# Optimization experiments

Measured on AMD Instinct MI355X. Metric: run time of the kernel, lower is better.

The kernel has to match this reference:

```python
import jax, jax.numpy as jnp
import numpy as np

N = 1024      # nodes == subgraphs (NGNN: one subgraph per node)
DEG = 8       # average degree
E = N * DEG   # edges
IND = 32      # indim
OUTD = 32     # outdim


def setup_inputs() -> dict:
    key = jax.random.key(0)
    k0, k1, k2, k3, k4 = jax.random.split(key, 5)
    X = jax.random.normal(k0, (N, N, IND), dtype=jnp.float32)
    # binary tuple-support mask (which (i,j) tuples exist in the sparse 2D tensor)
    mask = jax.random.randint(k1, (N, N), 0, 2).astype(jnp.int32)
    # adjacency edge list: A[row, col] = 1 (structure-only sparse adjacency)
    edge_row = jax.random.randint(k2, (E,), 0, N)  # destination j
    edge_col = jax.random.randint(k3, (E,), 0, N)  # source k
    # MLP (single linear layer, PygHO MLP default)
    W = jax.random.normal(k4, (IND, OUTD), dtype=jnp.float32) / np.sqrt(IND).astype(np.float32)
    b = jnp.zeros((OUTD,), dtype=jnp.float32)
    return {"X": X, "mask": mask, "edge_row": edge_row, "edge_col": edge_col, "W": W, "b": b}


def reference(X, mask, edge_row, edge_col, W, b):
    n = X.shape[0]
    m = mask.astype(X.dtype)[..., None]                      # [n, n, 1]
    # tuplewise MLP on existing tuples: tX[i,j] = X[i,j] @ W + b
    tX = (jnp.einsum("ijd,de->ije", X, W) + b) * m           # [n, n, OUTD]
    # message passing within each subgraph i along node dim j:
    # ret[i, j] = sum_{k : A[j,k]=1} tX[i, k]
    msgs = jnp.take(tX, edge_col, axis=1)                    # [n, E, OUTD] gather sources
    msgs = jnp.moveaxis(msgs, 1, 0)                          # [E, n, OUTD]
    agg = jax.ops.segment_sum(msgs, edge_row, num_segments=n)  # [j, i, OUTD]
    ret = jnp.swapaxes(agg, 0, 1) * m                        # restrict to tuple support (tarX = tX)
    return ret
```

## Files before the change

### kernel.cpp

```cpp
#include <hip/hip_runtime.h>


#define NN   1024
#define IND  32
#define OUTD 32

__global__ __launch_bounds__(1024) void k_zero(int* __restrict__ p, int n) {
    const int t = blockIdx.x * 1024 + threadIdx.x;
    if (t < n) p[t] = 0;
}

__global__ __launch_bounds__(1024) void k_count(const int* __restrict__ erow,
                                                int* __restrict__ cnt, int n_edges) {
    const int e = blockIdx.x * 1024 + threadIdx.x;
    if (e < n_edges) atomicAdd(&cnt[erow[e]], 1);
}

__global__ __launch_bounds__(1024) void k_scan(const int* __restrict__ cnt,
                                               int* __restrict__ row_ptr,
                                               int* __restrict__ fill) {
    __shared__ int sb[NN];
    const int t = threadIdx.x;
    const int v = cnt[t];
    sb[t] = v;
    __syncthreads();
    #pragma unroll
    for (int off = 1; off < NN; off <<= 1) {
        const int a = (t >= off) ? sb[t - off] : 0;
        __syncthreads();
        sb[t] += a;
        __syncthreads();
    }
    const int excl = sb[t] - v;
    row_ptr[t] = excl;
    fill[t]    = excl;
    if (t == NN - 1) row_ptr[NN] = sb[t];
}

__global__ __launch_bounds__(1024) void k_scatter(const int* __restrict__ erow,
                                                  const int* __restrict__ ecol,
                                                  int* __restrict__ fill,
                                                  int* __restrict__ cols, int n_edges) {
    const int e = blockIdx.x * 1024 + threadIdx.x;
    if (e < n_edges) {
        const int pos = atomicAdd(&fill[erow[e]], 1);
        cols[pos] = ecol[e];
    }
}

__global__ __launch_bounds__(1024) void ngnn_main_kernel(
    const float* __restrict__ X, const int* __restrict__ mask,
    const float* __restrict__ W, const float* __restrict__ b,
    const int* __restrict__ row_ptr, const int* __restrict__ cols,
    float* __restrict__ out)
{
    extern __shared__ float smem[];
    float* Xl    = smem;
    int*   maskl = (int*)(smem + NN * IND);

    const int t = threadIdx.x;
    const int i = blockIdx.x;

    maskl[t] = mask[(size_t)i * NN + t];

    const float4* Xg = (const float4*)(X + (size_t)i * NN * IND);
    #pragma unroll
    for (int it = 0; it < 8; ++it) {
        const int f4 = it * 1024 + t;
        const float4 v = Xg[f4];
        const int k = f4 >> 3;
        const int p = (f4 & 7) ^ (k & 7);
        *(float4*)(Xl + k * IND + (p << 2)) = v;
    }
    __syncthreads();

    const int j = t;
    float4* orow = (float4*)(out + ((size_t)i * NN + j) * OUTD);

    if (maskl[j] == 0) {
        const float4 z = {0.f, 0.f, 0.f, 0.f};
        #pragma unroll
        for (int q = 0; q < 8; ++q) orow[q] = z;
        return;
    }

    float S[IND];
    #pragma unroll
    for (int d = 0; d < IND; ++d) S[d] = 0.f;
    float cntf = 0.f;

    const int e0 = row_ptr[j];
    const int e1 = row_ptr[j + 1];
    for (int e = e0; e < e1; ++e) {
        const int k = cols[e];
        if (maskl[k]) {
            cntf += 1.f;
            const float* rb = Xl + k * IND;
            const int kb = k & 7;
            #pragma unroll
            for (int s = 0; s < 8; ++s) {
                const float4 v = *(const float4*)(rb + (((s ^ kb) << 2)));
                S[s * 4 + 0] += v.x;
                S[s * 4 + 1] += v.y;
                S[s * 4 + 2] += v.z;
                S[s * 4 + 3] += v.w;
            }
        }
    }

    float o[OUTD];
    #pragma unroll
    for (int c = 0; c < OUTD; ++c) o[c] = b[c] * cntf;
    #pragma unroll
    for (int d = 0; d < IND; ++d) {
        const float s = S[d];
        #pragma unroll
        for (int c = 0; c < OUTD; ++c) o[c] += s * W[d * OUTD + c];
    }

    #pragma unroll
    for (int q = 0; q < 8; ++q) {
        const float4 ov = { o[q*4+0], o[q*4+1], o[q*4+2], o[q*4+3] };
        orow[q] = ov;
    }
}

extern "C" void kernel_launch(void* const* d_in, const int* in_sizes, int n_in,
                              void* d_out, int out_size, void* d_ws, size_t ws_size,
                              hipStream_t stream) {
    const float* X    = (const float*)d_in[0];
    const int*   mask = (const int*)d_in[1];
    const int*   erow = (const int*)d_in[2];
    const int*   ecol = (const int*)d_in[3];
    const float* W    = (const float*)d_in[4];
    const float* b    = (const float*)d_in[5];
    float*       out  = (float*)d_out;

    const int n_edges = in_sizes[2];

    int* cnt     = (int*)d_ws;
    int* row_ptr = cnt + 1024;
    int* fill    = cnt + 2560;
    int* cols    = cnt + 4096;

    const int eb = (n_edges + 1023) / 1024;
    k_zero   <<<1, 1024, 0, stream>>>(cnt, NN);
    k_count  <<<eb, 1024, 0, stream>>>(erow, cnt, n_edges);
    k_scan   <<<1, 1024, 0, stream>>>(cnt, row_ptr, fill);
    k_scatter<<<eb, 1024, 0, stream>>>(erow, ecol, fill, cols, n_edges);

    const size_t shmem = (size_t)NN * IND * sizeof(float) + NN * sizeof(int);
    hipFuncSetAttribute((const void*)ngnn_main_kernel,
                        hipFuncAttributeMaxDynamicSharedMemorySize, (int)shmem);
    ngnn_main_kernel<<<NN, 1024, shmem, stream>>>(X, mask, W, b, row_ptr, cols, out);
}
```

Measured before the change: 309.7 us.

## Compact masked rows into shared memory and degree-sort output rows

The main kernel now uses a ballot-based prefix to compact only the masked-in source rows of X into shared memory, up to a cap of 560 slots, and falls back to global loads for any overflow. This cuts global reads and shared footprint for roughly half the rows. The scan kernel also produces a degree-bucketed ordering of destination nodes, so each wave handles rows of similar degree and masked-out rows form contiguous zero-writing tails, which reduces divergence. The W projection is vectorised with float4 loads, and the fill array reuses the count buffer. The fixed cap and shared-memory size assume the mask density stays near one half, and the shared footprint stays at about 77 KB.

```diff
diff --git a/kernel.cpp b/kernel.cpp
--- a/kernel.cpp
+++ b/kernel.cpp
@@ -4,6 +4,7 @@
 #define NN   1024
 #define IND  32
 #define OUTD 32
+#define CAP  560
 
 __global__ __launch_bounds__(1024) void k_zero(int* __restrict__ p, int n) {
     const int t = blockIdx.x * 1024 + threadIdx.x;
@@ -16,13 +17,17 @@
     if (e < n_edges) atomicAdd(&cnt[erow[e]], 1);
 }
 
-__global__ __launch_bounds__(1024) void k_scan(const int* __restrict__ cnt,
-                                               int* __restrict__ row_ptr,
-                                               int* __restrict__ fill) {
+__global__ __launch_bounds__(1024) void k_scan_sort(const int* __restrict__ cnt,
+                                                    int* __restrict__ row_ptr,
+                                                    int* __restrict__ fill,
+                                                    int* __restrict__ jorder) {
     __shared__ int sb[NN];
+    __shared__ int hist[64];
+    __shared__ int hoff[64];
     const int t = threadIdx.x;
     const int v = cnt[t];
     sb[t] = v;
+    if (t < 64) hist[t] = 0;
     __syncthreads();
     #pragma unroll
     for (int off = 1; off < NN; off <<= 1) {
@@ -35,6 +40,16 @@
     row_ptr[t] = excl;
     fill[t]    = excl;
     if (t == NN - 1) row_ptr[NN] = sb[t];
+    const int bkt = v < 63 ? v : 63;
+    atomicAdd(&hist[bkt], 1);
+    __syncthreads();
+    if (t == 0) {
+        int s = 0;
+        for (int q = 0; q < 64; ++q) { hoff[q] = s; s += hist[q]; }
+    }
+    __syncthreads();
+    const int pos = atomicAdd(&hoff[bkt], 1);
+    jorder[pos] = t;
 }
 
 __global__ __launch_bounds__(1024) void k_scatter(const int* __restrict__ erow,
@@ -48,36 +63,83 @@
     }
 }
 
-__global__ __launch_bounds__(1024) void ngnn_main_kernel(
+#define SMEM_BYTES 77248
+
+__global__ __launch_bounds__(1024, 8) void ngnn_main_kernel(
     const float* __restrict__ X, const int* __restrict__ mask,
     const float* __restrict__ W, const float* __restrict__ b,
     const int* __restrict__ row_ptr, const int* __restrict__ cols,
+    const int* __restrict__ jorder,
     float* __restrict__ out)
 {
     extern __shared__ float smem[];
-    float* Xl    = smem;
-    int*   maskl = (int*)(smem + NN * IND);
-
-    const int t = threadIdx.x;
-    const int i = blockIdx.x;
-
-    maskl[t] = mask[(size_t)i * NN + t];
-
-    const float4* Xg = (const float4*)(X + (size_t)i * NN * IND);
-    #pragma unroll
-    for (int it = 0; it < 8; ++it) {
-        const int f4 = it * 1024 + t;
-        const float4 v = Xg[f4];
-        const int k = f4 >> 3;
-        const int p = (f4 & 7) ^ (k & 7);
-        *(float4*)(Xl + k * IND + (p << 2)) = v;
-    }
-    __syncthreads();
-
-    const int j = t;
-    float4* orow = (float4*)(out + ((size_t)i * NN + j) * OUTD);
-
-    if (maskl[j] == 0) {
+    float*          Xl       = smem;
+    short*          slot_map = (short*)((char*)smem + 71680);
+    short*          sk       = (short*)((char*)smem + 73728);
+    unsigned short* jl       = (unsigned short*)((char*)smem + 74880);
+    int*            scr      = (int*)((char*)smem + 76928);
+    int* wt    = scr;
+    int* woff  = scr + 16;
+    int* wt2   = scr + 32;
+    int* woff2 = scr + 48;
+    int* RjS   = scr + 64;
+
+    const int t    = threadIdx.x;
+    const int i    = blockIdx.x;
+    const int w    = t >> 6;
+    const int lane = t & 63;
+    const unsigned long long ltmask = (lane == 63) ? 0x7fffffffffffffffull
+                                                   : ((1ull << lane) - 1ull);
+
+    const int mk = mask[(size_t)i * NN + t];
+    const int jj = jorder[t];
+    const unsigned long long bal = __ballot(mk != 0);
+    const int rank = __popcll(bal & ltmask);
+    if (lane == 0) wt[w] = __popcll(bal);
+    __syncthreads();
+    if (t == 0) {
+        int s = 0;
+        #pragma unroll
+        for (int q = 0; q < 16; ++q) { woff[q] = s; s += wt[q]; }
+    }
+    __syncthreads();
+    int slot = -2;
+    if (mk) { slot = woff[w] + rank; if (slot >= CAP) slot = -1; }
+    slot_map[t] = (short)slot;
+    if (slot >= 0) sk[slot] = (short)t;
+    const int R = woff[15] + wt[15];
+    __syncthreads();
+
+    const int mj = (slot_map[jj] != -2);
+    const unsigned long long bal2 = __ballot(mj);
+    const int rank2 = __popcll(bal2 & ltmask);
+    if (lane == 0) wt2[w] = __popcll(bal2);
+    __syncthreads();
+    if (t == 0) {
+        int s = 0;
+        #pragma unroll
+        for (int q = 0; q < 16; ++q) { woff2[q] = s; s += wt2[q]; }
+        *RjS = s;
+    }
+    __syncthreads();
+    const int Rj = *RjS;
+    if (mj) jl[woff2[w] + rank2] = (unsigned short)jj;
+    else    jl[Rj + (64 * w - woff2[w]) + (lane - rank2)] = (unsigned short)jj;
+
+    const int Rcap = R < CAP ? R : CAP;
+    const float4* Xg4 = (const float4*)(X + (size_t)i * NN * IND);
+    for (int idx = t; idx < Rcap * 8; idx += 1024) {
+        const int s = idx >> 3, q = idx & 7;
+        const int k = sk[s];
+        const float4 v = Xg4[k * 8 + q];
+        *(float4*)(Xl + s * IND + ((q ^ (s & 7)) << 2)) = v;
+    }
+    __syncthreads();
+
+    const int jv = jl[t];
+    float4* orow = (float4*)(out + ((size_t)i * NN + jv) * OUTD);
+
+    if (t >= Rj) {
         const float4 z = {0.f, 0.f, 0.f, 0.f};
         #pragma unroll
         for (int q = 0; q < 8; ++q) orow[q] = z;
@@ -89,39 +151,47 @@
     for (int d = 0; d < IND; ++d) S[d] = 0.f;
     float cntf = 0.f;
 
-    const int e0 = row_ptr[j];
-    const int e1 = row_ptr[j + 1];
+    const int e0 = row_ptr[jv];
+    const int e1 = row_ptr[jv + 1];
     for (int e = e0; e < e1; ++e) {
         const int k = cols[e];
-        if (maskl[k]) {
+        const int s = slot_map[k];
+        if (s >= 0) {
             cntf += 1.f;
-            const float* rb = Xl + k * IND;
-            const int kb = k & 7;
+            const float* rb = Xl + s * IND;
+            const int sx = (s & 7) << 2;
             #pragma unroll
-            for (int s = 0; s < 8; ++s) {
-                const float4 v = *(const float4*)(rb + (((s ^ kb) << 2)));
-                S[s * 4 + 0] += v.x;
-                S[s * 4 + 1] += v.y;
-                S[s * 4 + 2] += v.z;
-                S[s * 4 + 3] += v.w;
+            for (int q = 0; q < 8; ++q) {
+                const float4 v = *(const float4*)(rb + ((q << 2) ^ sx));
+                S[q * 4 + 0] += v.x; S[q * 4 + 1] += v.y;
+                S[q * 4 + 2] += v.z; S[q * 4 + 3] += v.w;
+            }
+        } else if (s == -1) {
+            cntf += 1.f;
+            const float4* xr = (const float4*)(X + ((size_t)i * NN + k) * IND);
+            #pragma unroll
+            for (int q = 0; q < 8; ++q) {
+                const float4 v = xr[q];
+                S[q * 4 + 0] += v.x; S[q * 4 + 1] += v.y;
+                S[q * 4 + 2] += v.z; S[q * 4 + 3] += v.w;
             }
         }
     }
 
-    float o[OUTD];
+    const float4* W4 = (const float4*)W;
+    const float4* b4 = (const float4*)b;
     #pragma unroll
-    for (int c = 0; c < OUTD; ++c) o[c] = b[c] * cntf;
-    #pragma unroll
-    for (int d = 0; d < IND; ++d) {
-        const float s = S[d];
-        #pragma unroll
-        for (int c = 0; c < OUTD; ++c) o[c] += s * W[d * OUTD + c];
-    }
-
-    #pragma unroll
-    for (int q = 0; q < 8; ++q) {
-        const float4 ov = { o[q*4+0], o[q*4+1], o[q*4+2], o[q*4+3] };
-        orow[q] = ov;
+    for (int g = 0; g < 8; ++g) {
+        const float4 bb = b4[g];
+        float4 acc = { bb.x * cntf, bb.y * cntf, bb.z * cntf, bb.w * cntf };
+        #pragma unroll
+        for (int d = 0; d < IND; ++d) {
+            const float4 wv = W4[d * 8 + g];
+            const float s = S[d];
+            acc.x += s * wv.x; acc.y += s * wv.y;
+            acc.z += s * wv.z; acc.w += s * wv.w;
+        }
+        orow[g] = acc;
     }
 }
 
@@ -138,19 +208,19 @@
 
     const int n_edges = in_sizes[2];
 
-    int* cnt     = (int*)d_ws;
-    int* row_ptr = cnt + 1024;
-    int* fill    = cnt + 2560;
-    int* cols    = cnt + 4096;
+    int* row_ptr = (int*)d_ws;
+    int* cnt     = row_ptr + 1088;
+    int* jorder  = row_ptr + 2112;
+    int* cols    = row_ptr + 3136;
 
     const int eb = (n_edges + 1023) / 1024;
-    k_zero   <<<1, 1024, 0, stream>>>(cnt, NN);
-    k_count  <<<eb, 1024, 0, stream>>>(erow, cnt, n_edges);
-    k_scan   <<<1, 1024, 0, stream>>>(cnt, row_ptr, fill);
-    k_scatter<<<eb, 1024, 0, stream>>>(erow, ecol, fill, cols, n_edges);
-
-    const size_t shmem = (size_t)NN * IND * sizeof(float) + NN * sizeof(int);
+    k_zero     <<<1, 1024, 0, stream>>>(cnt, NN);
+    k_count    <<<eb, 1024, 0, stream>>>(erow, cnt, n_edges);
+    k_scan_sort<<<1, 1024, 0, stream>>>(cnt, row_ptr, cnt , jorder);
+    k_scatter  <<<eb, 1024, 0, stream>>>(erow, ecol, cnt, cols, n_edges);
+
     hipFuncSetAttribute((const void*)ngnn_main_kernel,
-                        hipFuncAttributeMaxDynamicSharedMemorySize, (int)shmem);
-    ngnn_main_kernel<<<NN, 1024, shmem, stream>>>(X, mask, W, b, row_ptr, cols, out);
-}
+                        hipFuncAttributeMaxDynamicSharedMemorySize, SMEM_BYTES);
+    ngnn_main_kernel<<<NN, 1024, SMEM_BYTES, stream>>>(X, mask, W, b,
+                                                       row_ptr, cols, jorder, out);
+}
```

Result: slower. 438.8 us (+41.7%).
